# Performance work log

Hardware: AMD Instinct MI355X
Metric: run time of the kernel (lower is better)

Reference implementation:

```python
import jax, jax.numpy as jnp
import numpy as np

B, S, D, R, N_IN, N_PROC, K = 4, 4096, 1024, 128, 8, 32, 4

def setup_inputs() -> dict:
    key = jax.random.key(0)
    k1, k2, k3, k4, k5 = jax.random.split(key, 5)
    x = jax.random.normal(k1, (B, S, D), dtype=jnp.float32)
    input_weights = jax.random.uniform(k2, (B, S, N_IN), dtype=jnp.float32)
    process_indices = jax.random.randint(k3, (B, S, K), 0, N_PROC, dtype=jnp.int32)
    # params: orthogonal-ish init approximated by scaled gaussian
    input_neurons = jax.random.normal(k4, (N_IN, D, R), dtype=jnp.float32) / np.sqrt(D).astype(np.float32)
    process_neurons = jax.random.normal(k5, (N_PROC, R), dtype=jnp.float32)
    process_neurons = process_neurons / (jnp.linalg.norm(process_neurons, axis=-1, keepdims=True) + 1e-8)
    return {"x": x, "input_weights": input_weights, "process_indices": process_indices,
            "input_neurons": input_neurons, "process_neurons": process_neurons}

def reference(x, input_weights, process_indices, input_neurons, process_neurons):
    # soft routing over input neurons: project with all N_IN matrices, weight, sum
    all_proj = jnp.einsum('bsd,ndr->bsnr', x, input_neurons)      # [B,S,N_IN,R]
    y = jnp.einsum('bsnr,bsn->bsr', all_proj, input_weights)       # [B,S,R]
    # gather per-token Householder vectors: [B,S,K,R]
    selected_v = process_neurons[process_indices]
    # sequential chain of K Householder reflections via scan over the K axis
    def step(xc, v):
        # v: [B,S,R]
        v_norm_sq = jnp.sum(v * v, axis=-1, keepdims=True) + 1e-8
        vn = v / jnp.sqrt(v_norm_sq)
        vTx = jnp.sum(xc * vn, axis=-1, keepdims=True)
        return xc - 2.0 * vn * vTx, None
    out, _ = jax.lax.scan(step, y, jnp.moveaxis(selected_v, 2, 0))
    return out
```

## Files before the change

kernel.cpp:

```cpp
#include <hip/hip_runtime.h>
#include <hip/hip_bf16.h>
#include <stdint.h>

#define D_DIM 1024
#define R_DIM 128
#define NIN   8
#define M_TOT 16384

typedef unsigned short u16;
typedef __attribute__((ext_vector_type(4))) float f32x4;
typedef __attribute__((ext_vector_type(8))) __bf16 bf16x8;

__device__ __forceinline__ u16 f2b(float f) {
    union { float f; uint32_t u; } v; v.f = f;
    uint32_t r = (v.u + 0x7FFFu + ((v.u >> 16) & 1u)) >> 16;
    return (u16)r;
}

__device__ __forceinline__ void gload16(const void* g, void* l) {
    __builtin_amdgcn_global_load_lds(
        (const __attribute__((address_space(1))) uint32_t*)g,
        (__attribute__((address_space(3))) uint32_t*)l, 16, 0, 0);
}

__global__ __launch_bounds__(256)
void prep_x(const float* __restrict__ x, u16* __restrict__ xb) {
    const size_t i = ((size_t)blockIdx.x * 256 + threadIdx.x) * 8;
    const f32x4 v0 = *(const f32x4*)&x[i];
    const f32x4 v1 = *(const f32x4*)&x[i + 4];
    union { u16 s[8]; uint4 v; } u;
#pragma unroll
    for (int q = 0; q < 4; ++q) { u.s[q] = f2b(v0[q]); u.s[4 + q] = f2b(v1[q]); }
    *(uint4*)&xb[i] = u.v;
}

__global__ __launch_bounds__(128)
void prep_b(const float* __restrict__ inn, u16* __restrict__ Bt2) {
    const int n  = blockIdx.x;
    const int d0 = blockIdx.y * 64;
    const int r  = threadIdx.x;
    const size_t C = (size_t)((r >> 4) * 128 + n * 16 + (r & 15));
#pragma unroll
    for (int g = 0; g < 8; ++g) {
        union { u16 s[8]; uint4 v; } u;
#pragma unroll
        for (int jj = 0; jj < 8; ++jj)
            u.s[jj] = f2b(inn[((size_t)n * D_DIM + d0 + g * 8 + jj) * R_DIM + r]);
        *(uint4*)&Bt2[C * D_DIM + d0 + g * 8] = u.v;
    }
}

__global__ __launch_bounds__(256, 4)
void gemm_fused(const u16* __restrict__ xb, const u16* __restrict__ Bt2,
                const float* __restrict__ iw, float* __restrict__ y) {
    __shared__ __align__(16) u16 As[128 * 64];
    __shared__ __align__(16) u16 Bs[128 * 64];
    __shared__ __align__(16) float wsm[128 * 8];

    const int tid  = threadIdx.x;
    const int wid  = tid >> 6, lane = tid & 63;
    const int wr = wid >> 1, wc = wid & 1;
    const int l15 = lane & 15, lq = lane >> 4;

    int wg = (int)blockIdx.x;
    wg = (wg & 7) * 128 + (wg >> 3);
    const int by = wg & 7;
    const int bx = wg >> 3;
    const int m0 = bx * 128;
    const int c0 = by * 128;

    *(f32x4*)&wsm[tid * 4] = *(const f32x4*)&iw[(size_t)m0 * NIN + tid * 4];

    const int srow = tid >> 3;
    const int sby  = (tid & 7) * 16;
    const int sxor = sby ^ ((srow & 7) << 4);
    const char* gA = (const char*)xb  + ((size_t)(m0 + srow) * D_DIM) * 2 + sxor;
    const char* gB = (const char*)Bt2 + ((size_t)(c0 + srow) * D_DIM) * 2 + sxor;

    f32x4 acc[4][4] = {};

    for (int ks = 0; ks < 16; ++ks) {
        const int doff = ks * 128;
#pragma unroll
        for (int p = 0; p < 4; ++p) {
            gload16(gA + (size_t)p * (32 * 2048) + doff, (char*)As + p * 4096 + tid * 16);
            gload16(gB + (size_t)p * (32 * 2048) + doff, (char*)Bs + p * 4096 + tid * 16);
        }
        __syncthreads();

#pragma unroll
        for (int kk = 0; kk < 2; ++kk) {
            const uint32_t kbyte = (uint32_t)(kk * 64 + lq * 16);
            bf16x8 a[4], b[4];
#pragma unroll
            for (int i = 0; i < 4; ++i) {
                const int row = wr * 64 + i * 16 + l15;
                uint32_t off = (uint32_t)(row * 128) + kbyte;
                off ^= (uint32_t)((row & 7) << 4);
                a[i] = *(const bf16x8*)((const char*)As + off);
            }
#pragma unroll
            for (int i = 0; i < 4; ++i) {
                const int cc = wc * 64 + i * 16 + l15;
                uint32_t off = (uint32_t)(cc * 128) + kbyte;
                off ^= (uint32_t)((cc & 7) << 4);
                b[i] = *(const bf16x8*)((const char*)Bs + off);
            }
#pragma unroll
            for (int i = 0; i < 4; ++i)
#pragma unroll
                for (int j = 0; j < 4; ++j)
                    acc[i][j] = __builtin_amdgcn_mfma_f32_16x16x32_bf16(a[i], b[j], acc[i][j], 0, 0, 0);
        }
        __syncthreads();
    }

    float own[4][4];
#pragma unroll
    for (int i = 0; i < 4; ++i)
#pragma unroll
        for (int e = 0; e < 4; ++e) {
            const int row = wr * 64 + i * 16 + lq * 4 + e;
            float s = 0.f;
#pragma unroll
            for (int j = 0; j < 4; ++j)
                s += wsm[row * NIN + wc * 4 + j] * acc[i][j][e];
            own[i][e] = s;
        }

    float* pr = (float*)As;
    if (wc == 1) {
#pragma unroll
        for (int i = 0; i < 4; ++i)
#pragma unroll
            for (int e = 0; e < 4; ++e) {
                const int row = wr * 64 + i * 16 + lq * 4 + e;
                pr[row * 17 + l15] = own[i][e];
            }
    }
    __syncthreads();
    if (wc == 0) {
#pragma unroll
        for (int i = 0; i < 4; ++i)
#pragma unroll
            for (int e = 0; e < 4; ++e) {
                const int row = wr * 64 + i * 16 + lq * 4 + e;
                const float s = own[i][e] + pr[row * 17 + l15];
                y[(size_t)(m0 + row) * R_DIM + by * 16 + l15] = s;
            }
    }
}

__global__ __launch_bounds__(512)
void house(float* __restrict__ y, const int* __restrict__ pidx,
           const float* __restrict__ pn) {
    const int tid = threadIdx.x;
    const int row = tid >> 3;
    const int cg  = tid & 7;
    const int c0  = cg * 16;
    const int tok = blockIdx.x * 64 + row;

    float yv[16];
#pragma unroll
    for (int q = 0; q < 4; ++q) {
        const f32x4 s = *(const f32x4*)&y[(size_t)tok * R_DIM + c0 + q * 4];
        yv[q * 4 + 0] = s[0]; yv[q * 4 + 1] = s[1]; yv[q * 4 + 2] = s[2]; yv[q * 4 + 3] = s[3];
    }

    const int4 idx4 = *(const int4*)&pidx[tok * 4];
    const int idxs[4] = { idx4.x, idx4.y, idx4.z, idx4.w };

#pragma unroll
    for (int k = 0; k < 4; ++k) {
        const float* vptr = &pn[(size_t)idxs[k] * R_DIM + c0];
        float v[16];
#pragma unroll
        for (int q = 0; q < 4; ++q) {
            const f32x4 vv4 = *(const f32x4*)&vptr[q * 4];
            v[q * 4 + 0] = vv4[0]; v[q * 4 + 1] = vv4[1];
            v[q * 4 + 2] = vv4[2]; v[q * 4 + 3] = vv4[3];
        }
        float vy = 0.f, vv = 0.f;
#pragma unroll
        for (int j = 0; j < 16; ++j) { vy += v[j] * yv[j]; vv += v[j] * v[j]; }
#pragma unroll
        for (int o = 1; o < 8; o <<= 1) {
            vy += __shfl_xor(vy, o);
            vv += __shfl_xor(vv, o);
        }
        const float s = 2.0f * vy / (vv + 1e-8f);
#pragma unroll
        for (int j = 0; j < 16; ++j) yv[j] -= s * v[j];
    }

#pragma unroll
    for (int q = 0; q < 4; ++q) {
        f32x4 o; o[0] = yv[q*4+0]; o[1] = yv[q*4+1]; o[2] = yv[q*4+2]; o[3] = yv[q*4+3];
        *(f32x4*)&y[(size_t)tok * R_DIM + c0 + q * 4] = o;
    }
}

extern "C" void kernel_launch(void* const* d_in, const int* in_sizes, int n_in,
                              void* d_out, int out_size, void* d_ws, size_t ws_size,
                              hipStream_t stream) {
    const float* x   = (const float*)d_in[0];
    const float* iw  = (const float*)d_in[1];
    const int*   pix = (const int*)d_in[2];
    const float* inn = (const float*)d_in[3];
    const float* pn  = (const float*)d_in[4];
    float* out = (float*)d_out;

    u16* xb  = (u16*)d_ws;
    u16* Bt2 = (u16*)((char*)d_ws + (size_t)(32 << 20));

    prep_x<<<8192, 256, 0, stream>>>(x, xb);
    prep_b<<<dim3(8, 16), 128, 0, stream>>>(inn, Bt2);
    gemm_fused<<<1024, 256, 0, stream>>>(xb, Bt2, iw, out);
    house<<<256, 512, 0, stream>>>(out, pix, pn);
}
```

Measured before the change: 64.14 us.

## Double-buffer 256x256 bf16 GEMM with interleaved loads and merge prep kernels

Replaces the 128x128 single-buffered GEMM with a 256x256-tile, 8-wave kernel using 128KB of LDS double buffering. Next-tile global-to-LDS loads are interleaved with MFMA phases through explicit barriers, vmcnt waits and setprio. The two prep kernels become one launch, and the cross-wave reduction over input-neuron weights runs as a three-stage LDS accumulation. The goal is to hide load latency and raise reuse per tile. The cost is only 256 workgroups with one block per CU from the LDS size, and fragile hand-written wait counts.

```diff
diff --git a/kernel.cpp b/kernel.cpp
--- a/kernel.cpp
+++ b/kernel.cpp
@@ -23,132 +23,195 @@
         (__attribute__((address_space(3))) uint32_t*)l, 16, 0, 0);
 }
 
+#define SBAR do { asm volatile("" ::: "memory"); __builtin_amdgcn_s_barrier(); asm volatile("" ::: "memory"); } while (0)
+#define WVM4 asm volatile("s_waitcnt vmcnt(4)" ::: "memory")
+
 __global__ __launch_bounds__(256)
-void prep_x(const float* __restrict__ x, u16* __restrict__ xb) {
-    const size_t i = ((size_t)blockIdx.x * 256 + threadIdx.x) * 8;
-    const f32x4 v0 = *(const f32x4*)&x[i];
-    const f32x4 v1 = *(const f32x4*)&x[i + 4];
-    union { u16 s[8]; uint4 v; } u;
-#pragma unroll
-    for (int q = 0; q < 4; ++q) { u.s[q] = f2b(v0[q]); u.s[4 + q] = f2b(v1[q]); }
-    *(uint4*)&xb[i] = u.v;
-}
-
-__global__ __launch_bounds__(128)
-void prep_b(const float* __restrict__ inn, u16* __restrict__ Bt2) {
-    const int n  = blockIdx.x;
-    const int d0 = blockIdx.y * 64;
-    const int r  = threadIdx.x;
-    const size_t C = (size_t)((r >> 4) * 128 + n * 16 + (r & 15));
-#pragma unroll
-    for (int g = 0; g < 8; ++g) {
+void prep(const float* __restrict__ x, u16* __restrict__ xb,
+          const float* __restrict__ inn, u16* __restrict__ Bt2) {
+    if (blockIdx.x < 8192) {
+        const size_t i = ((size_t)blockIdx.x * 256 + threadIdx.x) * 8;
+        const f32x4 v0 = *(const f32x4*)&x[i];
+        const f32x4 v1 = *(const f32x4*)&x[i + 4];
         union { u16 s[8]; uint4 v; } u;
 #pragma unroll
-        for (int jj = 0; jj < 8; ++jj)
-            u.s[jj] = f2b(inn[((size_t)n * D_DIM + d0 + g * 8 + jj) * R_DIM + r]);
-        *(uint4*)&Bt2[C * D_DIM + d0 + g * 8] = u.v;
-    }
-}
-
-__global__ __launch_bounds__(256, 4)
-void gemm_fused(const u16* __restrict__ xb, const u16* __restrict__ Bt2,
-                const float* __restrict__ iw, float* __restrict__ y) {
-    __shared__ __align__(16) u16 As[128 * 64];
-    __shared__ __align__(16) u16 Bs[128 * 64];
-    __shared__ __align__(16) float wsm[128 * 8];
+        for (int q = 0; q < 4; ++q) { u.s[q] = f2b(v0[q]); u.s[4 + q] = f2b(v1[q]); }
+        *(uint4*)&xb[i] = u.v;
+    } else {
+        const int idx = (int)blockIdx.x - 8192;
+        const int n  = idx >> 4;
+        const int d0 = (idx & 15) * 64;
+        const int r   = threadIdx.x & 127;
+        const int hf  = threadIdx.x >> 7;
+        const size_t C = (size_t)((r >> 4) * 128 + n * 16 + (r & 15));
+#pragma unroll
+        for (int g = 0; g < 4; ++g) {
+            const int gg = hf * 4 + g;
+            union { u16 s[8]; uint4 v; } u;
+#pragma unroll
+            for (int jj = 0; jj < 8; ++jj)
+                u.s[jj] = f2b(inn[((size_t)n * D_DIM + d0 + gg * 8 + jj) * R_DIM + r]);
+            *(uint4*)&Bt2[C * D_DIM + d0 + gg * 8] = u.v;
+        }
+    }
+}
+
+__global__ __launch_bounds__(512, 2)
+void gemm8(const u16* __restrict__ xb, const u16* __restrict__ Bt2,
+           const float* __restrict__ iw, float* __restrict__ y) {
+    __shared__ __align__(16) char smem[131072];
+    char* As = smem;
+    char* Bs = smem + 65536;
 
     const int tid  = threadIdx.x;
     const int wid  = tid >> 6, lane = tid & 63;
-    const int wr = wid >> 1, wc = wid & 1;
+    const int wm = wid >> 2, wn = wid & 3;
     const int l15 = lane & 15, lq = lane >> 4;
 
     int wg = (int)blockIdx.x;
-    wg = (wg & 7) * 128 + (wg >> 3);
-    const int by = wg & 7;
-    const int bx = wg >> 3;
-    const int m0 = bx * 128;
-    const int c0 = by * 128;
-
-    *(f32x4*)&wsm[tid * 4] = *(const f32x4*)&iw[(size_t)m0 * NIN + tid * 4];
-
-    const int srow = tid >> 3;
-    const int sby  = (tid & 7) * 16;
-    const int sxor = sby ^ ((srow & 7) << 4);
-    const char* gA = (const char*)xb  + ((size_t)(m0 + srow) * D_DIM) * 2 + sxor;
-    const char* gB = (const char*)Bt2 + ((size_t)(c0 + srow) * D_DIM) * 2 + sxor;
-
-    f32x4 acc[4][4] = {};
-
-    for (int ks = 0; ks < 16; ++ks) {
-        const int doff = ks * 128;
-#pragma unroll
-        for (int p = 0; p < 4; ++p) {
-            gload16(gA + (size_t)p * (32 * 2048) + doff, (char*)As + p * 4096 + tid * 16);
-            gload16(gB + (size_t)p * (32 * 2048) + doff, (char*)Bs + p * 4096 + tid * 16);
-        }
-        __syncthreads();
-
-#pragma unroll
-        for (int kk = 0; kk < 2; ++kk) {
-            const uint32_t kbyte = (uint32_t)(kk * 64 + lq * 16);
-            bf16x8 a[4], b[4];
-#pragma unroll
-            for (int i = 0; i < 4; ++i) {
-                const int row = wr * 64 + i * 16 + l15;
-                uint32_t off = (uint32_t)(row * 128) + kbyte;
-                off ^= (uint32_t)((row & 7) << 4);
-                a[i] = *(const bf16x8*)((const char*)As + off);
+    wg = (wg & 7) * 32 + (wg >> 3);
+    const int by = wg & 3, bx = wg >> 2;
+    const int m0 = bx * 256, c0 = by * 256;
+
+    const int sxor = ((tid & 7) * 16) ^ (((tid >> 3) & 7) << 4);
+    const char* gA = (const char*)xb  + ((size_t)(m0 + (tid >> 3))) * 2048 + sxor;
+    const char* gB = (const char*)Bt2 + ((size_t)(c0 + (tid >> 3))) * 2048 + sxor;
+
+#define STA(T1, NB, Q) gload16(gA + (size_t)(Q) * 64 * 2048 + (size_t)(T1) * 128, As + (NB) * 32768 + (Q) * 8192 + tid * 16)
+#define STB(T1, NB, C) gload16(gB + (size_t)(C) * 64 * 2048 + (size_t)(T1) * 128, Bs + (NB) * 32768 + (C) * 8192 + tid * 16)
+
+#define RDA(DST, MH, CUR) \
+    _Pragma("unroll") for (int i = 0; i < 4; ++i) \
+    _Pragma("unroll") for (int kk = 0; kk < 2; ++kk) { \
+        const int row = wm * 128 + (MH) * 64 + i * 16 + l15; \
+        uint32_t off = (uint32_t)((CUR) * 32768 + row * 128 + kk * 64 + lq * 16); \
+        off ^= (uint32_t)((row & 7) << 4); \
+        DST[i][kk] = *(const bf16x8*)(As + off); }
+
+#define RDB(NS, CUR) \
+    _Pragma("unroll") for (int j = 0; j < 2; ++j) \
+    _Pragma("unroll") for (int kk = 0; kk < 2; ++kk) { \
+        const int cc = (NS) * 128 + wn * 32 + j * 16 + l15; \
+        uint32_t off = (uint32_t)((CUR) * 32768 + cc * 128 + kk * 64 + lq * 16); \
+        off ^= (uint32_t)((cc & 7) << 4); \
+        b[NS][j][kk] = *(const bf16x8*)(Bs + off); }
+
+#define MM(MH, NS, AF) do { \
+    __builtin_amdgcn_s_setprio(1); \
+    _Pragma("unroll") for (int i = 0; i < 4; ++i) \
+    _Pragma("unroll") for (int j = 0; j < 2; ++j) \
+    _Pragma("unroll") for (int kk = 0; kk < 2; ++kk) \
+        acc[MH][NS][i][j] = __builtin_amdgcn_mfma_f32_16x16x32_bf16(AF[i][kk], b[NS][j][kk], acc[MH][NS][i][j], 0, 0, 0); \
+    __builtin_amdgcn_s_setprio(0); } while (0)
+
+    f32x4 acc[2][2][4][2] = {};
+
+    STA(0, 0, 0); STA(0, 0, 2);
+    STB(0, 0, 0); STB(0, 0, 1);
+    STB(0, 0, 2); STB(0, 0, 3);
+    STA(0, 0, 1); STA(0, 0, 3);
+    WVM4; SBAR;
+
+    for (int t = 0; t < 16; ++t) {
+        const int cur = t & 1, nb = cur ^ 1;
+        const int t1 = t + 1;
+        const bool st = (t1 < 16);
+        bf16x8 a0[4][2], a1[4][2], b[2][2][2];
+
+        RDA(a0, 0, cur);
+        RDB(0, cur);
+        if (st) { STA(t1, nb, 0); STA(t1, nb, 2); }
+        SBAR;
+        MM(0, 0, a0);
+        WVM4; SBAR;
+
+        RDB(1, cur);
+        if (st) { STB(t1, nb, 0); STB(t1, nb, 1); }
+        SBAR;
+        MM(0, 1, a0);
+        WVM4; SBAR;
+
+        RDA(a1, 1, cur);
+        if (st) { STB(t1, nb, 2); STB(t1, nb, 3); }
+        SBAR;
+        MM(1, 0, a1);
+        SBAR;
+
+        if (st) { STA(t1, nb, 1); STA(t1, nb, 3); }
+        SBAR;
+        MM(1, 1, a1);
+        WVM4; SBAR;
+    }
+
+    float* P0 = (float*)smem;
+    float* P1 = (float*)(smem + 34816);
+    const float* wrow = iw + (size_t)m0 * NIN;
+
+    float own[2][2][4][4];
+#pragma unroll
+    for (int mh = 0; mh < 2; ++mh)
+#pragma unroll
+        for (int i = 0; i < 4; ++i)
+#pragma unroll
+            for (int e = 0; e < 4; ++e) {
+                const int row = wm * 128 + mh * 64 + i * 16 + lq * 4 + e;
+                const float w0 = wrow[row * NIN + wn * 2 + 0];
+                const float w1 = wrow[row * NIN + wn * 2 + 1];
+#pragma unroll
+                for (int ns = 0; ns < 2; ++ns)
+                    own[mh][ns][i][e] = w0 * acc[mh][ns][i][0][e] + w1 * acc[mh][ns][i][1][e];
             }
-#pragma unroll
-            for (int i = 0; i < 4; ++i) {
-                const int cc = wc * 64 + i * 16 + l15;
-                uint32_t off = (uint32_t)(cc * 128) + kbyte;
-                off ^= (uint32_t)((cc & 7) << 4);
-                b[i] = *(const bf16x8*)((const char*)Bs + off);
-            }
-#pragma unroll
-            for (int i = 0; i < 4; ++i)
-#pragma unroll
-                for (int j = 0; j < 4; ++j)
-                    acc[i][j] = __builtin_amdgcn_mfma_f32_16x16x32_bf16(a[i], b[j], acc[i][j], 0, 0, 0);
-        }
-        __syncthreads();
-    }
-
-    float own[4][4];
-#pragma unroll
-    for (int i = 0; i < 4; ++i)
-#pragma unroll
-        for (int e = 0; e < 4; ++e) {
-            const int row = wr * 64 + i * 16 + lq * 4 + e;
-            float s = 0.f;
-#pragma unroll
-            for (int j = 0; j < 4; ++j)
-                s += wsm[row * NIN + wc * 4 + j] * acc[i][j][e];
-            own[i][e] = s;
-        }
-
-    float* pr = (float*)As;
-    if (wc == 1) {
-#pragma unroll
-        for (int i = 0; i < 4; ++i)
-#pragma unroll
-            for (int e = 0; e < 4; ++e) {
-                const int row = wr * 64 + i * 16 + lq * 4 + e;
-                pr[row * 17 + l15] = own[i][e];
-            }
-    }
-    __syncthreads();
-    if (wc == 0) {
-#pragma unroll
-        for (int i = 0; i < 4; ++i)
-#pragma unroll
-            for (int e = 0; e < 4; ++e) {
-                const int row = wr * 64 + i * 16 + lq * 4 + e;
-                const float s = own[i][e] + pr[row * 17 + l15];
-                y[(size_t)(m0 + row) * R_DIM + by * 16 + l15] = s;
-            }
-    }
+
+#define PIX(NS, ROW) ((NS) * (256 * 17) + (ROW) * 17 + l15)
+    if (wn == 1 || wn == 3) {
+        float* P = (wn == 1) ? P0 : P1;
+#pragma unroll
+        for (int mh = 0; mh < 2; ++mh)
+#pragma unroll
+            for (int ns = 0; ns < 2; ++ns)
+#pragma unroll
+                for (int i = 0; i < 4; ++i)
+#pragma unroll
+                    for (int e = 0; e < 4; ++e) {
+                        const int row = wm * 128 + mh * 64 + i * 16 + lq * 4 + e;
+                        P[PIX(ns, row)] = own[mh][ns][i][e];
+                    }
+    }
+    SBAR;
+    if (wn == 2) {
+#pragma unroll
+        for (int mh = 0; mh < 2; ++mh)
+#pragma unroll
+            for (int ns = 0; ns < 2; ++ns)
+#pragma unroll
+                for (int i = 0; i < 4; ++i)
+#pragma unroll
+                    for (int e = 0; e < 4; ++e) {
+                        const int row = wm * 128 + mh * 64 + i * 16 + lq * 4 + e;
+                        P1[PIX(ns, row)] += own[mh][ns][i][e];
+                    }
+    }
+    SBAR;
+    if (wn == 0) {
+#pragma unroll
+        for (int mh = 0; mh < 2; ++mh)
+#pragma unroll
+            for (int ns = 0; ns < 2; ++ns)
+#pragma unroll
+                for (int i = 0; i < 4; ++i)
+#pragma unroll
+                    for (int e = 0; e < 4; ++e) {
+                        const int row = wm * 128 + mh * 64 + i * 16 + lq * 4 + e;
+                        const float s = own[mh][ns][i][e] + P0[PIX(ns, row)] + P1[PIX(ns, row)];
+                        y[(size_t)(m0 + row) * R_DIM + (2 * by + ns) * 16 + l15] = s;
+                    }
+    }
+#undef PIX
+#undef MM
+#undef RDB
+#undef RDA
+#undef STB
+#undef STA
 }
 
 __global__ __launch_bounds__(512)
@@ -213,8 +276,7 @@
     u16* xb  = (u16*)d_ws;
     u16* Bt2 = (u16*)((char*)d_ws + (size_t)(32 << 20));
 
-    prep_x<<<8192, 256, 0, stream>>>(x, xb);
-    prep_b<<<dim3(8, 16), 128, 0, stream>>>(inn, Bt2);
-    gemm_fused<<<1024, 256, 0, stream>>>(xb, Bt2, iw, out);
+    prep<<<8320, 256, 0, stream>>>(x, xb, inn, Bt2);
+    gemm8<<<256, 512, 0, stream>>>(xb, Bt2, iw, out);
     house<<<256, 512, 0, stream>>>(out, pix, pn);
 }
```

After: 66.35 us. +3.4%, slower.
